# Kernel tuning notes

Hardware: AMD Instinct MI355X
Metric: run time of the kernel (lower is better)

Reference implementation:

```python
import jax, jax.numpy as jnp
import numpy as np

N = 50000      # nodes
E = 400000     # edges (before self-loops)
IN = 128       # in_channels
OUT = 64       # out_channels (per-head; concat=False averages heads)
HEADS = 8      # heads of first GAT layer; second layer has 1 head
NEG_SLOPE = 0.2


def _glorot(key, shape, fan_in, fan_out):
    s = jnp.sqrt(2.0 / (fan_in + fan_out)).astype(jnp.float32)
    return jax.random.normal(key, shape, jnp.float32) * s


def setup_inputs() -> dict:
    key = jax.random.key(0)
    ks = jax.random.split(key, 10)
    x = jax.random.normal(ks[0], (N, IN), jnp.float32)
    edge_index = jax.random.randint(ks[1], (2, E), 0, N)
    # layer 1: heads=HEADS, per-head dim OUT
    W1 = _glorot(ks[2], (IN, HEADS * OUT), IN, HEADS * OUT)
    att_src1 = _glorot(ks[3], (HEADS, OUT), OUT, 1)
    att_dst1 = _glorot(ks[4], (HEADS, OUT), OUT, 1)
    b1 = jnp.zeros((OUT,), jnp.float32)
    # layer 2: heads=1
    W2 = _glorot(ks[5], (OUT, 1 * OUT), OUT, OUT)
    att_src2 = _glorot(ks[6], (1, OUT), OUT, 1)
    att_dst2 = _glorot(ks[7], (1, OUT), OUT, 1)
    b2 = jnp.zeros((OUT,), jnp.float32)
    return dict(x=x, edge_index=edge_index, W1=W1, att_src1=att_src1,
                att_dst1=att_dst1, b1=b1, W2=W2, att_src2=att_src2,
                att_dst2=att_dst2, b2=b2)


def gat_conv(x, edge_index, W, att_src, att_dst, bias, heads, ch):
    """PyG GATConv with concat=False (mean over heads), add_self_loops=True."""
    n = x.shape[0]
    loop = jnp.arange(n, dtype=edge_index.dtype)
    src = jnp.concatenate([edge_index[0], loop])  # [E+N]
    dst = jnp.concatenate([edge_index[1], loop])
    h = (x @ W).reshape(n, heads, ch)                     # [N, H, C]
    a_s = jnp.sum(h * att_src, axis=-1)                   # [N, H]
    a_d = jnp.sum(h * att_dst, axis=-1)                   # [N, H]
    e = jax.nn.leaky_relu(a_s[src] + a_d[dst], NEG_SLOPE)  # [E+N, H]
    # numerically stable segment softmax over incoming edges of each dst node
    emax = jax.lax.stop_gradient(
        jax.ops.segment_max(e, dst, num_segments=n))       # [N, H]
    ee = jnp.exp(e - emax[dst])
    denom = jax.ops.segment_sum(ee, dst, num_segments=n)  # [N, H]
    alpha = ee / denom[dst]                                # [E+N, H]
    out = jax.ops.segment_sum(alpha[:, :, None] * h[src], dst,
                              num_segments=n)              # [N, H, C]
    return out.mean(axis=1) + bias                         # [N, C]


def reference(x, edge_index, W1, att_src1, att_dst1, b1,
              W2, att_src2, att_dst2, b2):
    h = gat_conv(x, edge_index, W1, att_src1, att_dst1, b1, HEADS, OUT)
    h = jax.nn.elu(h)
    return gat_conv(h, edge_index, W2, att_src2, att_dst2, b2, 1, OUT)
```

## Files before the change

### kernel.cpp

```cpp
#include <hip/hip_runtime.h>
#include <cstdint>
#include <cstddef>

#define NEG_SLOPE 0.2f

typedef short bf16x8 __attribute__((ext_vector_type(8)));
typedef float f32x4 __attribute__((ext_vector_type(4)));
typedef float f32x2 __attribute__((ext_vector_type(2)));

__device__ __forceinline__ unsigned short f2bf(float f) {
  unsigned u = __float_as_uint(f);
  u = u + 0x7FFFu + ((u >> 16) & 1u);
  return (unsigned short)(u >> 16);
}
__device__ __forceinline__ float bf2f(unsigned short b) {
  return __uint_as_float((unsigned)b << 16);
}
__device__ __forceinline__ f32x2 unpk(unsigned xv) {
  f32x2 r;
  r.x = __uint_as_float(xv << 16);
  r.y = __uint_as_float(xv & 0xFFFF0000u);
  return r;
}
__device__ __forceinline__ float rlf(float v, int l) {
  return __uint_as_float(
      (unsigned)__builtin_amdgcn_readlane((int)__float_as_uint(v), l));
}
__device__ __forceinline__ void dma16(const unsigned short* g, unsigned short* l) {
  __builtin_amdgcn_global_load_lds(
      (const __attribute__((address_space(1))) unsigned*)g,
      (__attribute__((address_space(3))) unsigned*)l, 16, 0, 0);
}
__device__ __forceinline__ void dma4(const unsigned short* g, unsigned short* l) {
  __builtin_amdgcn_global_load_lds(
      (const __attribute__((address_space(1))) unsigned*)g,
      (__attribute__((address_space(3))) unsigned*)l, 4, 0, 0);
}

__global__ __launch_bounds__(256) void prep_all(
    const int* __restrict__ ei, int* __restrict__ counts,
    const float* __restrict__ x, unsigned short* __restrict__ xb,
    const float* __restrict__ W1, const float* __restrict__ att_s1,
    const float* __restrict__ att_d1, unsigned short* __restrict__ AsAdT,
    unsigned short* __restrict__ WbT,
    const float* __restrict__ W2, unsigned short* __restrict__ W2t,
    const float* __restrict__ att_s2, const float* __restrict__ att_d2,
    float* __restrict__ AsAd2,
    int E, int ET, int N, int B0, int B1) {
  int b = blockIdx.x, tid = threadIdx.x;
  if (b < B0) {
    int i = b * 256 + tid;
    if (i < ET) {
      int dst = (i < E) ? ei[E + i] : (i - E);
      atomicAdd(&counts[dst], 1);
    }
    return;
  }
  b -= B0;
  if (b < B1) {
    int i = b * 256 + tid;
    if (i < N * 32) {
      float4 v = ((const float4*)x)[i];
      ushort4 o;
      o.x = f2bf(v.x); o.y = f2bf(v.y); o.z = f2bf(v.z); o.w = f2bf(v.w);
      ((ushort4*)xb)[i] = o;
    }
    return;
  }
  b -= B1;
  if (b < 8) {
    int i = b * 256 + tid;
    int o = i >> 7, k = i & 127, h = o & 7;
    const float* att = (o < 8) ? att_s1 : att_d1;
    float s = 0.f;
    for (int c = 0; c < 64; c++) s += W1[(size_t)k * 512 + h * 64 + c] * att[h * 64 + c];
    AsAdT[i] = f2bf(s);
    return;
  }
  b -= 8;
  if (b < 256) {
    int i = b * 256 + tid;
    int o = i >> 10, k = i & 1023, h = k >> 7, c = k & 127;
    WbT[i] = f2bf(W1[(size_t)c * 512 + h * 64 + o]);
    return;
  }
  b -= 256;
  if (b < 16) {
    int i = b * 256 + tid;
    if (i < 64 * 64) {
      int k = i >> 6, nn = i & 63;
      W2t[(size_t)nn * 64 + k] = f2bf(W2[i]);
    }
    return;
  }
  {
    int i = tid;
    if (i < 128) {
      int o = i >> 6, k = i & 63;
      const float* att = (o == 0) ? att_s2 : att_d2;
      float s = 0.f;
      for (int c = 0; c < 64; c++) s += W2[(size_t)k * 64 + c] * att[c];
      AsAd2[i] = s;
    }
  }
}

__global__ __launch_bounds__(1024) void scan_dots(
    const int* __restrict__ counts, int* __restrict__ offsets,
    const unsigned short* __restrict__ xb, const unsigned short* __restrict__ AsAdT,
    float* __restrict__ asd, int n) {
  if (blockIdx.x == 0) {
    __shared__ int sums[1024];
    int t = threadIdx.x;
    int chunk = (n + 1023) >> 10;
    int start = t * chunk;
    int end = min(start + chunk, n);
    int s = 0;
    for (int i = start; i < end; i++) s += counts[i];
    sums[t] = s;
    __syncthreads();
    for (int off = 1; off < 1024; off <<= 1) {
      int v = (t >= off) ? sums[t - off] : 0;
      __syncthreads();
      sums[t] += v;
      __syncthreads();
    }
    int run = sums[t] - s;
    for (int i = start; i < end; i++) { offsets[i] = run; run += counts[i]; }
    if (t == 1023) offsets[n] = sums[1023];
    return;
  }
  int tid = threadIdx.x;
  int wave = tid >> 6, lane = tid & 63;
  int q = lane >> 4, t = lane & 15;
  int row0 = (blockIdx.x - 1) * 256 + wave * 16;
  int arow = row0 + t; if (arow > n - 1) arow = n - 1;
  const bf16x8* aptr = (const bf16x8*)(xb + (size_t)arow * 128);
  const bf16x8* bptr = (const bf16x8*)(AsAdT + t * 128);
  f32x4 acc = (f32x4){0.f, 0.f, 0.f, 0.f};
  #pragma unroll
  for (int s = 0; s < 4; s++)
    acc = __builtin_amdgcn_mfma_f32_16x16x32_bf16(aptr[s * 4 + q], bptr[s * 4 + q],
                                                  acc, 0, 0, 0);
  #pragma unroll
  for (int r = 0; r < 4; r++) {
    int row = row0 + q * 4 + r;
    if (row < n) asd[row * 16 + t] = acc[r];
  }
}

__global__ __launch_bounds__(256) void fill_csr(
    const int* __restrict__ ei, const int* __restrict__ offsets,
    int* __restrict__ cursor, int* __restrict__ srcs, int E, int ET) {
  int i = blockIdx.x * 256 + threadIdx.x;
  if (i >= ET) return;
  int src, dst;
  if (i < E) { src = ei[i]; dst = ei[E + i]; } else { src = dst = i - E; }
  int pos = atomicAdd(&cursor[dst], 1);
  srcs[offsets[dst] + pos] = src;
}

__global__ __launch_bounds__(1024, 8) void agg1_gemm(
    const int* __restrict__ offsets, const int* __restrict__ srcs,
    const float* __restrict__ asd, const unsigned short* __restrict__ xb,
    const unsigned short* __restrict__ WbT, const float* __restrict__ b1,
    const float* __restrict__ AsAd2, unsigned short* __restrict__ zb,
    float* __restrict__ as2, float* __restrict__ ad2, int N) {
  __shared__ unsigned short sh[16 * 2048];
  int tid = threadIdx.x;
  int wv = tid >> 6, lane = tid & 63;
  int nb = blockIdx.x;
  {
    int node = nb * 16 + wv;
    unsigned short* stg = &sh[wv * 2048];
    #pragma unroll
    for (int z = 0; z < 4; z++)
      ((f32x4*)stg)[z * 64 + lane] = (f32x4){0.f, 0.f, 0.f, 0.f};
    __builtin_amdgcn_s_waitcnt(0xC07F);
    f32x2 acc[8];
    #pragma unroll
    for (int h = 0; h < 8; h++) acc[h] = (f32x2){0.f, 0.f};
    float wsl = 0.f;
    int beg = offsets[node], end = offsets[node + 1];
    int jl = end - 1;
    float adv = asd[(size_t)node * 16 + 8 + (lane & 7)];
    for (int cb = beg; cb < end; cb += 16) {
      int cnt = min(16, end - cb);
      int sAll = srcs[min(cb + (lane & 15), jl)];
      int swa = srcs[min(cb + (lane >> 3), jl)];
      int swb = srcs[min(cb + 8 + (lane >> 3), jl)];
      float asva = asd[(size_t)swa * 16 + (lane & 7)];
      float asvb = asd[(size_t)swb * 16 + (lane & 7)];
      #pragma unroll
      for (int k = 0; k < 16; k++) {
        if (k < cnt) {
          int se = __builtin_amdgcn_readlane(sAll, k);
          dma4(xb + (size_t)(unsigned)se * 128 + 2 * lane, stg + k * 128);
        }
      }
      float wa, wb = 0.f;
      {
        float v = asva + adv;
        v = (v > 0.f) ? v : NEG_SLOPE * v;
        wa = (cb + (lane >> 3) < end) ? __expf(v) : 0.f;
      }
      if (cnt > 8) {
        float v = asvb + adv;
        v = (v > 0.f) ? v : NEG_SLOPE * v;
        wb = (cb + 8 + (lane >> 3) < end) ? __expf(v) : 0.f;
      }
      wsl += wa + wb;
      __builtin_amdgcn_s_waitcnt(0x0f70);
      #pragma unroll
      for (int k = 0; k < 8; k++) {
        unsigned xv = *(const unsigned*)&stg[k * 128 + 2 * lane];
        f32x2 x2 = unpk(xv);
        acc[0] += x2 * rlf(wa, k * 8 + 0);
        acc[1] += x2 * rlf(wa, k * 8 + 1);
        acc[2] += x2 * rlf(wa, k * 8 + 2);
        acc[3] += x2 * rlf(wa, k * 8 + 3);
        acc[4] += x2 * rlf(wa, k * 8 + 4);
        acc[5] += x2 * rlf(wa, k * 8 + 5);
        acc[6] += x2 * rlf(wa, k * 8 + 6);
        acc[7] += x2 * rlf(wa, k * 8 + 7);
      }
      if (cnt > 8) {
        #pragma unroll
        for (int k = 0; k < 8; k++) {
          unsigned xv = *(const unsigned*)&stg[1024 + k * 128 + 2 * lane];
          f32x2 x2 = unpk(xv);
          acc[0] += x2 * rlf(wb, k * 8 + 0);
          acc[1] += x2 * rlf(wb, k * 8 + 1);
          acc[2] += x2 * rlf(wb, k * 8 + 2);
          acc[3] += x2 * rlf(wb, k * 8 + 3);
          acc[4] += x2 * rlf(wb, k * 8 + 4);
          acc[5] += x2 * rlf(wb, k * 8 + 5);
          acc[6] += x2 * rlf(wb, k * 8 + 6);
          acc[7] += x2 * rlf(wb, k * 8 + 7);
        }
      }
    }
    wsl += __shfl_xor(wsl, 8, 64);
    wsl += __shfl_xor(wsl, 16, 64);
    wsl += __shfl_xor(wsl, 32, 64);
    __syncthreads();
    #pragma unroll
    for (int h = 0; h < 8; h++) {
      float tot = rlf(wsl, h);
      float iv = 0.125f / tot;
      unsigned o = (unsigned)f2bf(acc[h].x * iv) | ((unsigned)f2bf(acc[h].y * iv) << 16);
      *(unsigned*)&sh[wv * 1032 + h * 128 + 2 * lane] = o;
    }
  }
  __syncthreads();
  if (wv < 4) {
    int q = lane >> 4, t = lane & 15;
    f32x4 acc4 = (f32x4){0.f, 0.f, 0.f, 0.f};
    const unsigned short* bbase = WbT + (size_t)(wv * 16 + t) * 1024;
    #pragma unroll 8
    for (int s = 0; s < 32; s++) {
      bf16x8 af = *(const bf16x8*)&sh[t * 1032 + s * 32 + q * 8];
      bf16x8 bf = *(const bf16x8*)&bbase[s * 32 + q * 8];
      acc4 = __builtin_amdgcn_mfma_f32_16x16x32_bf16(af, bf, acc4, 0, 0, 0);
    }
    int col = wv * 16 + t;
    float bias = b1[col];
    float vs = AsAd2[col], vd = AsAd2[64 + col];
    #pragma unroll
    for (int r = 0; r < 4; r++) {
      int row = q * 4 + r;
      int node = nb * 16 + row;
      float v = acc4[r] + bias;
      v = (v > 0.f) ? v : (__expf(v) - 1.f);
      zb[(size_t)node * 64 + col] = f2bf(v);
      float s = v * vs, d = v * vd;
      #pragma unroll
      for (int off = 1; off < 16; off <<= 1) {
        s += __shfl_xor(s, off, 64);
        d += __shfl_xor(d, off, 64);
      }
      if (t == 0) {
        atomicAdd(&as2[node], s);
        atomicAdd(&ad2[node], d);
      }
    }
  }
}

__global__ __launch_bounds__(1024, 8) void agg2_gemm(
    const int* __restrict__ offsets, const int* __restrict__ srcs,
    const float* __restrict__ as2, const float* __restrict__ ad2,
    const unsigned short* __restrict__ zb, const unsigned short* __restrict__ W2t,
    const float* __restrict__ b2, float* __restrict__ out, int N) {
  __shared__ unsigned short stg[16 * 1024];
  __shared__ unsigned short sh[16 * 72];
  int tid = threadIdx.x;
  int wv = tid >> 6, lane = tid & 63;
  int nb = blockIdx.x;
  {
    int node = nb * 16 + wv;
    unsigned short* st = &stg[wv * 1024];
    #pragma unroll
    for (int z = 0; z < 2; z++)
      ((f32x4*)st)[z * 64 + lane] = (f32x4){0.f, 0.f, 0.f, 0.f};
    __builtin_amdgcn_s_waitcnt(0xC07F);
    float adv = ad2[node];
    int beg = offsets[node], end = offsets[node + 1];
    int jl = end - 1;
    f32x2 acc = (f32x2){0.f, 0.f};
    float wsl = 0.f;
    for (int cb = beg; cb < end; cb += 16) {
      int cnt = min(16, end - cb);
      int sAll = srcs[min(cb + (lane & 15), jl)];
      float asv = as2[sAll];
      #pragma unroll
      for (int k = 0; k < 8; k++) {
        if (2 * k < cnt) {
          int sa = __builtin_amdgcn_readlane(sAll, 2 * k);
          int sb = __builtin_amdgcn_readlane(sAll, 2 * k + 1);
          int se = (lane >= 32) ? sb : sa;
          dma4(zb + (size_t)(unsigned)se * 64 + 2 * (lane & 31), st + k * 128);
        }
      }
      float v = asv + adv;
      v = (v > 0.f) ? v : NEG_SLOPE * v;
      float wl = (cb + (lane & 15) < end) ? __expf(v) : 0.f;
      if (lane < 16) wsl += wl;
      __builtin_amdgcn_s_waitcnt(0x0f70);
      #pragma unroll
      for (int k = 0; k < 4; k++) {
        float w0 = rlf(wl, 2 * k);
        float w1 = rlf(wl, 2 * k + 1);
        float w = (lane >= 32) ? w1 : w0;
        unsigned zv = *(const unsigned*)&st[k * 128 + 2 * lane];
        acc += unpk(zv) * w;
      }
      if (cnt > 8) {
        #pragma unroll
        for (int k = 4; k < 8; k++) {
          float w0 = rlf(wl, 2 * k);
          float w1 = rlf(wl, 2 * k + 1);
          float w = (lane >= 32) ? w1 : w0;
          unsigned zv = *(const unsigned*)&st[k * 128 + 2 * lane];
          acc += unpk(zv) * w;
        }
      }
    }
    wsl += __shfl_xor(wsl, 1, 64);
    wsl += __shfl_xor(wsl, 2, 64);
    wsl += __shfl_xor(wsl, 4, 64);
    wsl += __shfl_xor(wsl, 8, 64);
    float tot = rlf(wsl, 0);
    acc.x += __shfl_xor(acc.x, 32, 64);
    acc.y += __shfl_xor(acc.y, 32, 64);
    if (lane < 32) {
      float inv = 1.f / tot;
      unsigned o = (unsigned)f2bf(acc.x * inv) | ((unsigned)f2bf(acc.y * inv) << 16);
      *(unsigned*)&sh[wv * 72 + 2 * lane] = o;
    }
  }
  __syncthreads();
  if (wv < 4) {
    int q = lane >> 4, t = lane & 15;
    f32x4 acc4 = (f32x4){0.f, 0.f, 0.f, 0.f};
    const unsigned short* bbase = W2t + (size_t)(wv * 16 + t) * 64;
    #pragma unroll
    for (int s = 0; s < 2; s++) {
      bf16x8 af = *(const bf16x8*)&sh[t * 72 + s * 32 + q * 8];
      bf16x8 bf = *(const bf16x8*)&bbase[s * 32 + q * 8];
      acc4 = __builtin_amdgcn_mfma_f32_16x16x32_bf16(af, bf, acc4, 0, 0, 0);
    }
    int col = wv * 16 + t;
    float bias = b2[col];
    #pragma unroll
    for (int r = 0; r < 4; r++) {
      int node = nb * 16 + q * 4 + r;
      if (node < N) out[(size_t)node * 64 + col] = acc4[r] + bias;
    }
  }
}

extern "C" void kernel_launch(void* const* d_in, const int* in_sizes, int n_in,
                              void* d_out, int out_size, void* d_ws, size_t ws_size,
                              hipStream_t stream) {
  const int IN = 128;
  const int N = in_sizes[0] / IN;
  const int E = in_sizes[1] / 2;
  const int ET = E + N;

  const float* x        = (const float*)d_in[0];
  const int*   ei       = (const int*)d_in[1];
  const float* W1       = (const float*)d_in[2];
  const float* att_src1 = (const float*)d_in[3];
  const float* att_dst1 = (const float*)d_in[4];
  const float* b1       = (const float*)d_in[5];
  const float* W2       = (const float*)d_in[6];
  const float* att_src2 = (const float*)d_in[7];
  const float* att_dst2 = (const float*)d_in[8];
  const float* b2       = (const float*)d_in[9];
  float* out = (float*)d_out;

  char* base = (char*)d_ws;
  size_t off = 0;
  auto alloc = [&](size_t bytes) -> char* {
    char* p = base + off;
    off = (off + bytes + 255) & ~(size_t)255;
    return p;
  };
  unsigned short* xb    = (unsigned short*)alloc((size_t)N * 128 * 2);
  unsigned short* AsAdT = (unsigned short*)alloc((size_t)16 * 128 * 2);
  unsigned short* WbT   = (unsigned short*)alloc((size_t)64 * 1024 * 2);
  unsigned short* W2t   = (unsigned short*)alloc((size_t)64 * 64 * 2);
  unsigned short* zb    = (unsigned short*)alloc((size_t)N * 64 * 2);
  float* AsAd2 = (float*)alloc((size_t)128 * 4);
  float* asd1  = (float*)alloc((size_t)N * 16 * 4);
  int* offsets = (int*)alloc((size_t)(N + 1) * 4);
  int* srcs    = (int*)alloc((size_t)ET * 4);
  char* zero_begin = base + off;
  int* counts  = (int*)alloc((size_t)N * 4);
  int* cursor  = (int*)alloc((size_t)N * 4);
  float* a_s2  = (float*)alloc((size_t)N * 4);
  float* a_d2  = (float*)alloc((size_t)N * 4);
  char* zero_end = base + off;

  hipMemsetAsync(zero_begin, 0, (size_t)(zero_end - zero_begin), stream);

  const int TB = 256;
  auto cdiv = [](int a, int b) { return (a + b - 1) / b; };

  int B0 = cdiv(ET, TB);
  int B1 = cdiv(N * 32, TB);
  prep_all<<<B0 + B1 + 8 + 256 + 16 + 1, TB, 0, stream>>>(
      ei, counts, x, xb, W1, att_src1, att_dst1, AsAdT, WbT, W2, W2t,
      att_src2, att_dst2, AsAd2, E, ET, N, B0, B1);

  scan_dots<<<1 + cdiv(N, 256), 1024, 0, stream>>>(counts, offsets, xb, AsAdT,
                                                   asd1, N);

  fill_csr<<<cdiv(ET, TB), TB, 0, stream>>>(ei, offsets, cursor, srcs, E, ET);

  agg1_gemm<<<cdiv(N, 16), 1024, 0, stream>>>(offsets, srcs, asd1, xb, WbT, b1,
                                              AsAd2, zb, a_s2, a_d2, N);

  agg2_gemm<<<cdiv(N, 16), 1024, 0, stream>>>(offsets, srcs, a_s2, a_d2, zb,
                                              W2t, b2, out, N);
}
```

Before: 347.7 us.

## Process two nodes per wave and gather rows with 16-byte LDS DMA

Both aggregation kernels now give each wavefront two destination nodes instead of one, using blocks of 512 threads rather than 1024, and interleave the neighbor gathers of both nodes. The per-edge 4-byte global-to-LDS loads are replaced by 16-byte loads that fetch several neighbor rows per instruction. The aim is fewer load instructions, more bytes in flight per wave, and overlap of one node's latency with the other's. The cost is higher register pressure from doubled accumulators, imbalance when the two nodes have different degrees, and the staging-buffer zeroing is removed.

```diff
diff --git a/kernel.cpp b/kernel.cpp
--- a/kernel.cpp
+++ b/kernel.cpp
@@ -30,11 +30,6 @@
   __builtin_amdgcn_global_load_lds(
       (const __attribute__((address_space(1))) unsigned*)g,
       (__attribute__((address_space(3))) unsigned*)l, 16, 0, 0);
-}
-__device__ __forceinline__ void dma4(const unsigned short* g, unsigned short* l) {
-  __builtin_amdgcn_global_load_lds(
-      (const __attribute__((address_space(1))) unsigned*)g,
-      (__attribute__((address_space(3))) unsigned*)l, 4, 0, 0);
 }
 
 __global__ __launch_bounds__(256) void prep_all(
@@ -160,7 +155,22 @@
   srcs[offsets[dst] + pos] = src;
 }
 
-__global__ __launch_bounds__(1024, 8) void agg1_gemm(
+#define CONSUME8(STG, W, ACC)                                         \
+  _Pragma("unroll")                                                   \
+  for (int k = 0; k < 8; k++) {                                       \
+    unsigned xv = *(const unsigned*)&(STG)[k * 128 + 2 * lane];       \
+    f32x2 x2 = unpk(xv);                                              \
+    ACC[0] += x2 * rlf(W, k * 8 + 0);                                 \
+    ACC[1] += x2 * rlf(W, k * 8 + 1);                                 \
+    ACC[2] += x2 * rlf(W, k * 8 + 2);                                 \
+    ACC[3] += x2 * rlf(W, k * 8 + 3);                                 \
+    ACC[4] += x2 * rlf(W, k * 8 + 4);                                 \
+    ACC[5] += x2 * rlf(W, k * 8 + 5);                                 \
+    ACC[6] += x2 * rlf(W, k * 8 + 6);                                 \
+    ACC[7] += x2 * rlf(W, k * 8 + 7);                                 \
+  }
+
+__global__ __launch_bounds__(512, 4) void agg1_gemm(
     const int* __restrict__ offsets, const int* __restrict__ srcs,
     const float* __restrict__ asd, const unsigned short* __restrict__ xb,
     const unsigned short* __restrict__ WbT, const float* __restrict__ b1,
@@ -171,85 +181,121 @@
   int wv = tid >> 6, lane = tid & 63;
   int nb = blockIdx.x;
   {
-    int node = nb * 16 + wv;
-    unsigned short* stg = &sh[wv * 2048];
+    int nodeA = nb * 16 + 2 * wv;
+    unsigned short* stgA = &sh[(2 * wv) * 2048];
+    unsigned short* stgB = &sh[(2 * wv + 1) * 2048];
+    f32x2 accA[8], accB[8];
     #pragma unroll
-    for (int z = 0; z < 4; z++)
-      ((f32x4*)stg)[z * 64 + lane] = (f32x4){0.f, 0.f, 0.f, 0.f};
-    __builtin_amdgcn_s_waitcnt(0xC07F);
-    f32x2 acc[8];
-    #pragma unroll
-    for (int h = 0; h < 8; h++) acc[h] = (f32x2){0.f, 0.f};
-    float wsl = 0.f;
-    int beg = offsets[node], end = offsets[node + 1];
-    int jl = end - 1;
-    float adv = asd[(size_t)node * 16 + 8 + (lane & 7)];
-    for (int cb = beg; cb < end; cb += 16) {
-      int cnt = min(16, end - cb);
-      int sAll = srcs[min(cb + (lane & 15), jl)];
-      int swa = srcs[min(cb + (lane >> 3), jl)];
-      int swb = srcs[min(cb + 8 + (lane >> 3), jl)];
-      float asva = asd[(size_t)swa * 16 + (lane & 7)];
-      float asvb = asd[(size_t)swb * 16 + (lane & 7)];
-      #pragma unroll
-      for (int k = 0; k < 16; k++) {
-        if (k < cnt) {
-          int se = __builtin_amdgcn_readlane(sAll, k);
-          dma4(xb + (size_t)(unsigned)se * 128 + 2 * lane, stg + k * 128);
-        }
-      }
-      float wa, wb = 0.f;
-      {
-        float v = asva + adv;
+    for (int h = 0; h < 8; h++) {
+      accA[h] = (f32x2){0.f, 0.f};
+      accB[h] = (f32x2){0.f, 0.f};
+    }
+    float wslA = 0.f, wslB = 0.f;
+    int begA = offsets[nodeA];
+    int endA = offsets[nodeA + 1];
+    int endB = offsets[nodeA + 2];
+    int begB = endA;
+    int jlA = endA - 1, jlB = endB - 1;
+    float advA = asd[(size_t)nodeA * 16 + 8 + (lane & 7)];
+    float advB = asd[(size_t)(nodeA + 1) * 16 + 8 + (lane & 7)];
+    for (int c = 0;; c += 16) {
+      int cbA = begA + c, cbB = begB + c;
+      bool hA = cbA < endA, hB = cbB < endB;
+      if (!hA && !hB) break;
+      int cntA = endA - cbA, cntB = endB - cbB;
+      int sA0 = 0, sA1 = 0, sA2 = 0, sA3 = 0;
+      int sB0 = 0, sB1 = 0, sB2 = 0, sB3 = 0;
+      float asvaA = 0.f, asvbA = 0.f, asvaB = 0.f, asvbB = 0.f;
+      if (hA) {
+        sA0 = srcs[min(cbA + (lane >> 4), jlA)];
+        sA1 = srcs[min(cbA + 4 + (lane >> 4), jlA)];
+        int sw = srcs[min(cbA + (lane >> 3), jlA)];
+        asvaA = asd[(size_t)sw * 16 + (lane & 7)];
+        if (cntA > 8) {
+          sA2 = srcs[min(cbA + 8 + (lane >> 4), jlA)];
+          sA3 = srcs[min(cbA + 12 + (lane >> 4), jlA)];
+          int sw2 = srcs[min(cbA + 8 + (lane >> 3), jlA)];
+          asvbA = asd[(size_t)sw2 * 16 + (lane & 7)];
+        }
+      }
+      if (hB) {
+        sB0 = srcs[min(cbB + (lane >> 4), jlB)];
+        sB1 = srcs[min(cbB + 4 + (lane >> 4), jlB)];
+        int sw = srcs[min(cbB + (lane >> 3), jlB)];
+        asvaB = asd[(size_t)sw * 16 + (lane & 7)];
+        if (cntB > 8) {
+          sB2 = srcs[min(cbB + 8 + (lane >> 4), jlB)];
+          sB3 = srcs[min(cbB + 12 + (lane >> 4), jlB)];
+          int sw2 = srcs[min(cbB + 8 + (lane >> 3), jlB)];
+          asvbB = asd[(size_t)sw2 * 16 + (lane & 7)];
+        }
+      }
+      if (hA) {
+        dma16(xb + (size_t)(unsigned)sA0 * 128 + (lane & 15) * 8, stgA);
+        dma16(xb + (size_t)(unsigned)sA1 * 128 + (lane & 15) * 8, stgA + 512);
+        if (cntA > 8) {
+          dma16(xb + (size_t)(unsigned)sA2 * 128 + (lane & 15) * 8, stgA + 1024);
+          dma16(xb + (size_t)(unsigned)sA3 * 128 + (lane & 15) * 8, stgA + 1536);
+        }
+      }
+      if (hB) {
+        dma16(xb + (size_t)(unsigned)sB0 * 128 + (lane & 15) * 8, stgB);
+        dma16(xb + (size_t)(unsigned)sB1 * 128 + (lane & 15) * 8, stgB + 512);
+        if (cntB > 8) {
+          dma16(xb + (size_t)(unsigned)sB2 * 128 + (lane & 15) * 8, stgB + 1024);
+          dma16(xb + (size_t)(unsigned)sB3 * 128 + (lane & 15) * 8, stgB + 1536);
+        }
+      }
+      float waA = 0.f, wbA = 0.f, waB = 0.f, wbB = 0.f;
+      if (hA) {
+        float v = asvaA + advA;
         v = (v > 0.f) ? v : NEG_SLOPE * v;
-        wa = (cb + (lane >> 3) < end) ? __expf(v) : 0.f;
-      }
-      if (cnt > 8) {
-        float v = asvb + adv;
+        waA = (cbA + (lane >> 3) < endA) ? __expf(v) : 0.f;
+        if (cntA > 8) {
+          v = asvbA + advA;
+          v = (v > 0.f) ? v : NEG_SLOPE * v;
+          wbA = (cbA + 8 + (lane >> 3) < endA) ? __expf(v) : 0.f;
+        }
+      }
+      if (hB) {
+        float v = asvaB + advB;
         v = (v > 0.f) ? v : NEG_SLOPE * v;
-        wb = (cb + 8 + (lane >> 3) < end) ? __expf(v) : 0.f;
-      }
-      wsl += wa + wb;
+        waB = (cbB + (lane >> 3) < endB) ? __expf(v) : 0.f;
+        if (cntB > 8) {
+          v = asvbB + advB;
+          v = (v > 0.f) ? v : NEG_SLOPE * v;
+          wbB = (cbB + 8 + (lane >> 3) < endB) ? __expf(v) : 0.f;
+        }
+      }
+      wslA += waA + wbA;
+      wslB += waB + wbB;
       __builtin_amdgcn_s_waitcnt(0x0f70);
-      #pragma unroll
-      for (int k = 0; k < 8; k++) {
-        unsigned xv = *(const unsigned*)&stg[k * 128 + 2 * lane];
-        f32x2 x2 = unpk(xv);
-        acc[0] += x2 * rlf(wa, k * 8 + 0);
-        acc[1] += x2 * rlf(wa, k * 8 + 1);
-        acc[2] += x2 * rlf(wa, k * 8 + 2);
-        acc[3] += x2 * rlf(wa, k * 8 + 3);
-        acc[4] += x2 * rlf(wa, k * 8 + 4);
-        acc[5] += x2 * rlf(wa, k * 8 + 5);
-        acc[6] += x2 * rlf(wa, k * 8 + 6);
-        acc[7] += x2 * rlf(wa, k * 8 + 7);
-      }
-      if (cnt > 8) {
-        #pragma unroll
-        for (int k = 0; k < 8; k++) {
-          unsigned xv = *(const unsigned*)&stg[1024 + k * 128 + 2 * lane];
-          f32x2 x2 = unpk(xv);
-          acc[0] += x2 * rlf(wb, k * 8 + 0);
-          acc[1] += x2 * rlf(wb, k * 8 + 1);
-          acc[2] += x2 * rlf(wb, k * 8 + 2);
-          acc[3] += x2 * rlf(wb, k * 8 + 3);
-          acc[4] += x2 * rlf(wb, k * 8 + 4);
-          acc[5] += x2 * rlf(wb, k * 8 + 5);
-          acc[6] += x2 * rlf(wb, k * 8 + 6);
-          acc[7] += x2 * rlf(wb, k * 8 + 7);
-        }
-      }
-    }
-    wsl += __shfl_xor(wsl, 8, 64);
-    wsl += __shfl_xor(wsl, 16, 64);
-    wsl += __shfl_xor(wsl, 32, 64);
+      if (hA) {
+        CONSUME8(stgA, waA, accA);
+        if (cntA > 8) { CONSUME8((stgA + 1024), wbA, accA); }
+      }
+      if (hB) {
+        CONSUME8(stgB, waB, accB);
+        if (cntB > 8) { CONSUME8((stgB + 1024), wbB, accB); }
+      }
+    }
+    wslA += __shfl_xor(wslA, 8, 64);
+    wslA += __shfl_xor(wslA, 16, 64);
+    wslA += __shfl_xor(wslA, 32, 64);
+    wslB += __shfl_xor(wslB, 8, 64);
+    wslB += __shfl_xor(wslB, 16, 64);
+    wslB += __shfl_xor(wslB, 32, 64);
     __syncthreads();
     #pragma unroll
     for (int h = 0; h < 8; h++) {
-      float tot = rlf(wsl, h);
-      float iv = 0.125f / tot;
-      unsigned o = (unsigned)f2bf(acc[h].x * iv) | ((unsigned)f2bf(acc[h].y * iv) << 16);
-      *(unsigned*)&sh[wv * 1032 + h * 128 + 2 * lane] = o;
+      float ivA = 0.125f / rlf(wslA, h);
+      unsigned oA = (unsigned)f2bf(accA[h].x * ivA) |
+                    ((unsigned)f2bf(accA[h].y * ivA) << 16);
+      *(unsigned*)&sh[(2 * wv) * 1032 + h * 128 + 2 * lane] = oA;
+      float ivB = 0.125f / rlf(wslB, h);
+      unsigned oB = (unsigned)f2bf(accB[h].x * ivB) |
+                    ((unsigned)f2bf(accB[h].y * ivB) << 16);
+      *(unsigned*)&sh[(2 * wv + 1) * 1032 + h * 128 + 2 * lane] = oB;
     }
   }
   __syncthreads();
@@ -287,7 +333,7 @@
   }
 }
 
-__global__ __launch_bounds__(1024, 8) void agg2_gemm(
+__global__ __launch_bounds__(512, 8) void agg2_gemm(
     const int* __restrict__ offsets, const int* __restrict__ srcs,
     const float* __restrict__ as2, const float* __restrict__ ad2,
     const unsigned short* __restrict__ zb, const unsigned short* __restrict__ W2t,
@@ -298,65 +344,124 @@
   int wv = tid >> 6, lane = tid & 63;
   int nb = blockIdx.x;
   {
-    int node = nb * 16 + wv;
-    unsigned short* st = &stg[wv * 1024];
-    #pragma unroll
-    for (int z = 0; z < 2; z++)
-      ((f32x4*)st)[z * 64 + lane] = (f32x4){0.f, 0.f, 0.f, 0.f};
-    __builtin_amdgcn_s_waitcnt(0xC07F);
-    float adv = ad2[node];
-    int beg = offsets[node], end = offsets[node + 1];
-    int jl = end - 1;
-    f32x2 acc = (f32x2){0.f, 0.f};
-    float wsl = 0.f;
-    for (int cb = beg; cb < end; cb += 16) {
-      int cnt = min(16, end - cb);
-      int sAll = srcs[min(cb + (lane & 15), jl)];
-      float asv = as2[sAll];
-      #pragma unroll
-      for (int k = 0; k < 8; k++) {
-        if (2 * k < cnt) {
-          int sa = __builtin_amdgcn_readlane(sAll, 2 * k);
-          int sb = __builtin_amdgcn_readlane(sAll, 2 * k + 1);
-          int se = (lane >= 32) ? sb : sa;
-          dma4(zb + (size_t)(unsigned)se * 64 + 2 * (lane & 31), st + k * 128);
-        }
-      }
-      float v = asv + adv;
-      v = (v > 0.f) ? v : NEG_SLOPE * v;
-      float wl = (cb + (lane & 15) < end) ? __expf(v) : 0.f;
-      if (lane < 16) wsl += wl;
+    int nodeA = nb * 16 + 2 * wv;
+    unsigned short* stA = &stg[(2 * wv) * 1024];
+    unsigned short* stB = &stg[(2 * wv + 1) * 1024];
+    f32x2 accA = (f32x2){0.f, 0.f}, accB = (f32x2){0.f, 0.f};
+    float wslA = 0.f, wslB = 0.f;
+    int begA = offsets[nodeA];
+    int endA = offsets[nodeA + 1];
+    int endB = offsets[nodeA + 2];
+    int begB = endA;
+    int jlA = endA - 1, jlB = endB - 1;
+    float advA = ad2[nodeA];
+    float advB = ad2[nodeA + 1];
+    for (int c = 0;; c += 16) {
+      int cbA = begA + c, cbB = begB + c;
+      bool hA = cbA < endA, hB = cbB < endB;
+      if (!hA && !hB) break;
+      int cntA = endA - cbA, cntB = endB - cbB;
+      float wlA = 0.f, wlB = 0.f;
+      int sR0A = 0, sR1A = 0, sR0B = 0, sR1B = 0;
+      float asvA = 0.f, asvB = 0.f;
+      if (hA) {
+        int sAll = srcs[min(cbA + (lane & 15), jlA)];
+        asvA = as2[sAll];
+        sR0A = srcs[min(cbA + (lane >> 3), jlA)];
+        if (cntA > 8) sR1A = srcs[min(cbA + 8 + (lane >> 3), jlA)];
+      }
+      if (hB) {
+        int sAll = srcs[min(cbB + (lane & 15), jlB)];
+        asvB = as2[sAll];
+        sR0B = srcs[min(cbB + (lane >> 3), jlB)];
+        if (cntB > 8) sR1B = srcs[min(cbB + 8 + (lane >> 3), jlB)];
+      }
+      if (hA) {
+        dma16(zb + (size_t)(unsigned)sR0A * 64 + (lane & 7) * 8, stA);
+        if (cntA > 8)
+          dma16(zb + (size_t)(unsigned)sR1A * 64 + (lane & 7) * 8, stA + 512);
+      }
+      if (hB) {
+        dma16(zb + (size_t)(unsigned)sR0B * 64 + (lane & 7) * 8, stB);
+        if (cntB > 8)
+          dma16(zb + (size_t)(unsigned)sR1B * 64 + (lane & 7) * 8, stB + 512);
+      }
+      if (hA) {
+        float v = asvA + advA;
+        v = (v > 0.f) ? v : NEG_SLOPE * v;
+        wlA = (cbA + (lane & 15) < endA) ? __expf(v) : 0.f;
+      }
+      if (hB) {
+        float v = asvB + advB;
+        v = (v > 0.f) ? v : NEG_SLOPE * v;
+        wlB = (cbB + (lane & 15) < endB) ? __expf(v) : 0.f;
+      }
+      if (lane < 16) { wslA += wlA; wslB += wlB; }
       __builtin_amdgcn_s_waitcnt(0x0f70);
-      #pragma unroll
-      for (int k = 0; k < 4; k++) {
-        float w0 = rlf(wl, 2 * k);
-        float w1 = rlf(wl, 2 * k + 1);
-        float w = (lane >= 32) ? w1 : w0;
-        unsigned zv = *(const unsigned*)&st[k * 128 + 2 * lane];
-        acc += unpk(zv) * w;
-      }
-      if (cnt > 8) {
+      if (hA) {
         #pragma unroll
-        for (int k = 4; k < 8; k++) {
-          float w0 = rlf(wl, 2 * k);
-          float w1 = rlf(wl, 2 * k + 1);
+        for (int k = 0; k < 4; k++) {
+          float w0 = rlf(wlA, 2 * k);
+          float w1 = rlf(wlA, 2 * k + 1);
           float w = (lane >= 32) ? w1 : w0;
-          unsigned zv = *(const unsigned*)&st[k * 128 + 2 * lane];
-          acc += unpk(zv) * w;
-        }
-      }
-    }
-    wsl += __shfl_xor(wsl, 1, 64);
-    wsl += __shfl_xor(wsl, 2, 64);
-    wsl += __shfl_xor(wsl, 4, 64);
-    wsl += __shfl_xor(wsl, 8, 64);
-    float tot = rlf(wsl, 0);
-    acc.x += __shfl_xor(acc.x, 32, 64);
-    acc.y += __shfl_xor(acc.y, 32, 64);
+          unsigned zv = *(const unsigned*)&stA[k * 128 + 2 * lane];
+          accA += unpk(zv) * w;
+        }
+        if (cntA > 8) {
+          #pragma unroll
+          for (int k = 4; k < 8; k++) {
+            float w0 = rlf(wlA, 2 * k);
+            float w1 = rlf(wlA, 2 * k + 1);
+            float w = (lane >= 32) ? w1 : w0;
+            unsigned zv = *(const unsigned*)&stA[k * 128 + 2 * lane];
+            accA += unpk(zv) * w;
+          }
+        }
+      }
+      if (hB) {
+        #pragma unroll
+        for (int k = 0; k < 4; k++) {
+          float w0 = rlf(wlB, 2 * k);
+          float w1 = rlf(wlB, 2 * k + 1);
+          float w = (lane >= 32) ? w1 : w0;
+          unsigned zv = *(const unsigned*)&stB[k * 128 + 2 * lane];
+          accB += unpk(zv) * w;
+        }
+        if (cntB > 8) {
+          #pragma unroll
+          for (int k = 4; k < 8; k++) {
+            float w0 = rlf(wlB, 2 * k);
+            float w1 = rlf(wlB, 2 * k + 1);
+            float w = (lane >= 32) ? w1 : w0;
+            unsigned zv = *(const unsigned*)&stB[k * 128 + 2 * lane];
+            accB += unpk(zv) * w;
+          }
+        }
+      }
+    }
+    wslA += __shfl_xor(wslA, 1, 64);
+    wslA += __shfl_xor(wslA, 2, 64);
+    wslA += __shfl_xor(wslA, 4, 64);
+    wslA += __shfl_xor(wslA, 8, 64);
+    wslB += __shfl_xor(wslB, 1, 64);
+    wslB += __shfl_xor(wslB, 2, 64);
+    wslB += __shfl_xor(wslB, 4, 64);
+    wslB += __shfl_xor(wslB, 8, 64);
+    float totA = rlf(wslA, 0);
+    float totB = rlf(wslB, 0);
+    accA.x += __shfl_xor(accA.x, 32, 64);
+    accA.y += __shfl_xor(accA.y, 32, 64);
+    accB.x += __shfl_xor(accB.x, 32, 64);
+    accB.y += __shfl_xor(accB.y, 32, 64);
     if (lane < 32) {
-      float inv = 1.f / tot;
-      unsigned o = (unsigned)f2bf(acc.x * inv) | ((unsigned)f2bf(acc.y * inv) << 16);
-      *(unsigned*)&sh[wv * 72 + 2 * lane] = o;
+      float invA = 1.f / totA;
+      unsigned oA = (unsigned)f2bf(accA.x * invA) |
+                    ((unsigned)f2bf(accA.y * invA) << 16);
+      *(unsigned*)&sh[(2 * wv) * 72 + 2 * lane] = oA;
+      float invB = 1.f / totB;
+      unsigned oB = (unsigned)f2bf(accB.x * invB) |
+                    ((unsigned)f2bf(accB.y * invB) << 16);
+      *(unsigned*)&sh[(2 * wv + 1) * 72 + 2 * lane] = oB;
     }
   }
   __syncthreads();
@@ -439,9 +544,9 @@
 
   fill_csr<<<cdiv(ET, TB), TB, 0, stream>>>(ei, offsets, cursor, srcs, E, ET);
 
-  agg1_gemm<<<cdiv(N, 16), 1024, 0, stream>>>(offsets, srcs, asd1, xb, WbT, b1,
-                                              AsAd2, zb, a_s2, a_d2, N);
-
-  agg2_gemm<<<cdiv(N, 16), 1024, 0, stream>>>(offsets, srcs, a_s2, a_d2, zb,
-                                              W2t, b2, out, N);
-}
+  agg1_gemm<<<cdiv(N, 16), 512, 0, stream>>>(offsets, srcs, asd1, xb, WbT, b1,
+                                             AsAd2, zb, a_s2, a_d2, N);
+
+  agg2_gemm<<<cdiv(N, 16), 512, 0, stream>>>(offsets, srcs, a_s2, a_d2, zb,
+                                             W2t, b2, out, N);
+}
```

After: 327.2 us. 1.06x faster.
